# Performance work log

Hardware: AMD Instinct MI355X
Metric: run time of the kernel (lower is better)

## Reference

```python
import jax, jax.numpy as jnp
import numpy as np

N_MODELS = 16
IN_F = 1024
OUT_F = 1024
N_TOK = 8192


def setup_inputs() -> dict:
    key = jax.random.key(0)
    k1, k2, k3, k4 = jax.random.split(key, 4)
    x = jax.random.normal(k1, (N_TOK, IN_F), dtype=jnp.float32)
    idxs = jax.random.randint(k2, (N_TOK,), 0, N_MODELS, dtype=jnp.int64)
    w = jax.random.normal(k3, (N_MODELS, IN_F, OUT_F), dtype=jnp.float32) * 0.02
    b = jax.random.normal(k4, (N_MODELS, OUT_F), dtype=jnp.float32) * 0.02
    return {"x": x, "idxs": idxs, "w": w, "b": b}


def reference(x, idxs, w, b):
    # Equivalent math to the torch loop: for each expert i, tokens with
    # idxs==i get x @ w[i] + b[i]; finally ReLU over all outputs.
    # Loop over the small fixed expert count; selection by mask avoids
    # materializing the [N, E, out] tensor or gathering per-token weights.
    y = jnp.zeros((x.shape[0], w.shape[2]), dtype=x.dtype)
    for i in range(w.shape[0]):
        yi = x @ w[i] + b[i]  # [N, out]
        y = jnp.where((idxs == i)[:, None], yi, y)
    return jax.nn.relu(y)
```

## Files before the change

### kernel.cpp

```cpp
#include <hip/hip_runtime.h>
#include <hip/hip_bf16.h>
#include <stdint.h>

#define N_MODELS 16
#define IN_F 1024
#define OUT_F 1024
#define N_TOK 8192
#define MAX_MT 80

typedef unsigned short u16;
using us4   = __attribute__((ext_vector_type(4))) unsigned short;
using s16x8 = __attribute__((ext_vector_type(8))) short;
using f32x4 = __attribute__((ext_vector_type(4))) float;

__device__ __forceinline__ u16 f2bf(float f) {
    union { float f; uint32_t u; } v;
    v.f = f;
    uint32_t u = v.u;
    u += 0x7fffu + ((u >> 16) & 1u);
    return (u16)(u >> 16);
}

__device__ __forceinline__ void gload16(const u16* g, u16* l) {
    __builtin_amdgcn_global_load_lds(
        (const __attribute__((address_space(1))) void*)g,
        (__attribute__((address_space(3))) void*)l, 16, 0, 0);
}

__global__ void bucket_kernel(const int* __restrict__ idxs,
                              int* __restrict__ perm,
                              int* __restrict__ offs,
                              int* __restrict__ tile_off)
{
    __shared__ int cnt[N_MODELS];
    __shared__ int cur[N_MODELS];
    int t = threadIdx.x;
    if (t < N_MODELS) cnt[t] = 0;
    __syncthreads();
    for (int i = t; i < N_TOK; i += 256) atomicAdd(&cnt[idxs[i]], 1);
    __syncthreads();
    if (t == 0) {
        int o = 0, to = 0;
        for (int e = 0; e < N_MODELS; ++e) {
            offs[e] = o; tile_off[e] = to; cur[e] = o;
            to += (cnt[e] + 127) / 128;
            o  += cnt[e];
        }
        offs[N_MODELS] = o; tile_off[N_MODELS] = to;
    }
    __syncthreads();
    for (int i = t; i < N_TOK; i += 256) {
        int e = idxs[i];
        int p = atomicAdd(&cur[e], 1);
        perm[p] = i;
    }
}

#define WBLOCKS (16*8*16)
#define SH_S 132

__global__ __launch_bounds__(256)
void prep_kernel(const float* __restrict__ w, const float* __restrict__ x,
                 const int* __restrict__ perm, const int* __restrict__ offs,
                 const int* __restrict__ tile_off,
                 u16* __restrict__ wT, u16* __restrict__ xg)
{
    __shared__ u16 sh[64 * SH_S];
    int t  = threadIdx.x;
    int bx = blockIdx.x;

    if (bx < WBLOCKS) {
        int e  = bx >> 7;
        int nt = (bx >> 4) & 7;
        int kg = bx & 15;
        const float* wp = w + (size_t)e * 1048576 + (size_t)kg * 65536 + nt * 128;
        int n4  = t & 31;
        int kr0 = t >> 5;
#pragma unroll
        for (int p = 0; p < 8; ++p) {
            int kr = kr0 + p * 8;
            const float4 v = *(const float4*)(wp + (size_t)kr * 1024 + n4 * 4);
            us4 pk; pk.x = f2bf(v.x); pk.y = f2bf(v.y); pk.z = f2bf(v.z); pk.w = f2bf(v.w);
            *(us4*)(&sh[kr * SH_S + n4 * 4]) = pk;
        }
        __syncthreads();
        int n  = t & 127;
        int qh = t >> 7;
        u16* outb = wT + ((size_t)(e * 8 + nt) * 32) * 4096;
#pragma unroll
        for (int oct = 0; oct < 4; ++oct) {
            int ko = qh + oct * 2;
            int kb = kg * 2 + (ko >> 2);
            int q  = ko & 3;
            s16x8 v;
#pragma unroll
            for (int j = 0; j < 8; ++j) v[j] = (short)sh[(ko * 8 + j) * SH_S + n];
            *(s16x8*)(outb + ((size_t)kb * 4 + q) * 1024 + n * 8) = v;
        }
    } else {
        int bx2 = bx - WBLOCKS;
        int mt = bx2 >> 3;
        int kg = bx2 & 7;
        int total = tile_off[16];
        if (mt >= total) return;
        int e = 0;
        while (tile_off[e + 1] <= mt) ++e;
        int s0   = offs[e] + (mt - tile_off[e]) * 128;
        int sEnd = offs[e + 1];
        int r0   = t >> 3;
        int apos = t & 7;
        int toks[4];
#pragma unroll
        for (int i = 0; i < 4; ++i) {
            int r = r0 + i * 32;
            toks[i] = (s0 + r < sEnd) ? perm[s0 + r] : -1;
        }
        u16* outx = xg + (size_t)mt * 32 * 4096;
        for (int kb4 = 0; kb4 < 4; ++kb4) {
            int kb = kg * 4 + kb4;
#pragma unroll
            for (int i = 0; i < 4; ++i) {
                int r = r0 + i * 32;
                int k = kb * 32 + apos * 4;
                float4 v;
                if (toks[i] >= 0) v = *(const float4*)(x + (size_t)toks[i] * 1024 + k);
                else              v = make_float4(0.f, 0.f, 0.f, 0.f);
                us4 pk; pk.x = f2bf(v.x); pk.y = f2bf(v.y); pk.z = f2bf(v.z); pk.w = f2bf(v.w);
                *(us4*)(&sh[(apos >> 1) * 1024 + r * 8 + (apos & 1) * 4]) = pk;
            }
            __syncthreads();
#pragma unroll
            for (int i = 0; i < 2; ++i) {
                int c = t + i * 256;
                *(s16x8*)(outx + (size_t)kb * 4096 + c * 8) = *(const s16x8*)(&sh[c * 8]);
            }
            __syncthreads();
        }
    }
}

__global__ __launch_bounds__(256)
void gemm_kernel(const u16* __restrict__ xg, const u16* __restrict__ wT,
                 const float* __restrict__ bias,
                 const int* __restrict__ perm, const int* __restrict__ offs,
                 const int* __restrict__ tile_off,
                 float* __restrict__ out)
{
    __shared__ u16 As[4096];
    __shared__ u16 Bs[4096];
    __shared__ int   permS[128];
    __shared__ float biasS[128];
    __shared__ int   toS[N_MODELS + 1];

    int t  = threadIdx.x;
    int bt = blockIdx.y;
    int nt = blockIdx.x;

    if (t <= N_MODELS) toS[t] = tile_off[t];
    __syncthreads();
    if (bt >= toS[N_MODELS]) return;

    int e = 0;
    while (toS[e + 1] <= bt) ++e;
    int s0   = offs[e] + (bt - toS[e]) * 128;
    int sEnd = offs[e + 1];
    int mValid = sEnd - s0; if (mValid > 128) mValid = 128;

    if (t < 128) {
        permS[t] = (s0 + t < sEnd) ? perm[s0 + t] : 0;
        biasS[t] = bias[(size_t)e * OUT_F + nt * 128 + t];
    }

    const u16* atile = xg + (size_t)bt * 32 * 4096;
    const u16* btile = wT + ((size_t)(e * 8 + nt) * 32) * 4096;

    int lane = t & 63;
    int wv   = t >> 6;
    int wm   = (wv >> 1) * 64;
    int wn   = (wv & 1) * 64;
    int m    = lane & 15;
    int q    = lane >> 4;

    f32x4 acc[4][4];
#pragma unroll
    for (int i = 0; i < 4; ++i)
#pragma unroll
        for (int j = 0; j < 4; ++j)
            acc[i][j] = (f32x4){0.f, 0.f, 0.f, 0.f};

    int c = wv * 2;

    for (int kb = 0; kb < 32; ++kb) {
        const u16* ga = atile + kb * 4096;
        const u16* gb = btile + kb * 4096;
        gload16(ga + (c    ) * 512 + lane * 8, &As[(c    ) * 512]);
        gload16(ga + (c + 1) * 512 + lane * 8, &As[(c + 1) * 512]);
        gload16(gb + (c    ) * 512 + lane * 8, &Bs[(c    ) * 512]);
        gload16(gb + (c + 1) * 512 + lane * 8, &Bs[(c + 1) * 512]);
        __syncthreads();

        s16x8 af[4], bf[4];
#pragma unroll
        for (int mt2 = 0; mt2 < 4; ++mt2)
            af[mt2] = *(const s16x8*)(&As[q * 1024 + (wm + mt2 * 16 + m) * 8]);
#pragma unroll
        for (int nt2 = 0; nt2 < 4; ++nt2)
            bf[nt2] = *(const s16x8*)(&Bs[q * 1024 + (wn + nt2 * 16 + m) * 8]);
#pragma unroll
        for (int mt2 = 0; mt2 < 4; ++mt2)
#pragma unroll
            for (int nt2 = 0; nt2 < 4; ++nt2)
                acc[mt2][nt2] = __builtin_amdgcn_mfma_f32_16x16x32_bf16(
                    af[mt2], bf[nt2], acc[mt2][nt2], 0, 0, 0);
        __syncthreads();
    }

#pragma unroll
    for (int mt2 = 0; mt2 < 4; ++mt2) {
        int rbase = wm + mt2 * 16 + q * 4;
#pragma unroll
        for (int i = 0; i < 4; ++i) {
            int r = rbase + i;
            if (r < mValid) {
                int tok = permS[r];
                float* orow = out + (size_t)tok * OUT_F + nt * 128;
#pragma unroll
                for (int nt2 = 0; nt2 < 4; ++nt2) {
                    int col = wn + nt2 * 16 + m;
                    float v = acc[mt2][nt2][i] + biasS[col];
                    orow[col] = v > 0.f ? v : 0.f;
                }
            }
        }
    }
}

extern "C" void kernel_launch(void* const* d_in, const int* in_sizes, int n_in,
                              void* d_out, int out_size, void* d_ws, size_t ws_size,
                              hipStream_t stream) {
    const float* x    = (const float*)d_in[0];
    const int*   idxs = (const int*)d_in[1];
    const float* w    = (const float*)d_in[2];
    const float* b    = (const float*)d_in[3];
    float* out = (float*)d_out;

    u16* wT = (u16*)d_ws;
    u16* xg = wT + (size_t)N_MODELS * IN_F * OUT_F;
    int* perm     = (int*)(xg + (size_t)MAX_MT * 32 * 4096);
    int* offs     = perm + N_TOK;
    int* tile_off = offs + (N_MODELS + 1);

    bucket_kernel<<<1, 256, 0, stream>>>(idxs, perm, offs, tile_off);
    prep_kernel<<<WBLOCKS + 640, 256, 0, stream>>>(w, x, perm, offs, tile_off, wT, xg);
    gemm_kernel<<<dim3(8, MAX_MT), 256, 0, stream>>>(xg, wT, b, perm, offs, tile_off, out);
}
```

Before: 194.5 us.

## Parallelize token bucketing and split weight/activation prep into separate kernels

The single-block bucketing kernel is replaced by a multi-block histogram, a one-thread scan, and a multi-block atomic scatter, spreading the token bucketing across many blocks. The combined prep kernel is split into a weight-conversion kernel, which now reads columns directly without an LDS transpose, and a separate activation-gather kernel. This removes serialization on a single block but adds several extra kernel launches and a memset. The direct strided weight reads may also be less coalesced than the old staged transpose.

```diff
diff --git a/kernel.cpp b/kernel.cpp
--- a/kernel.cpp
+++ b/kernel.cpp
@@ -27,115 +27,103 @@
         (__attribute__((address_space(3))) void*)l, 16, 0, 0);
 }
 
-__global__ void bucket_kernel(const int* __restrict__ idxs,
-                              int* __restrict__ perm,
-                              int* __restrict__ offs,
-                              int* __restrict__ tile_off)
-{
+__global__ void hist_kernel(const int* __restrict__ idxs, int* __restrict__ ghist) {
     __shared__ int cnt[N_MODELS];
-    __shared__ int cur[N_MODELS];
     int t = threadIdx.x;
     if (t < N_MODELS) cnt[t] = 0;
     __syncthreads();
-    for (int i = t; i < N_TOK; i += 256) atomicAdd(&cnt[idxs[i]], 1);
+    int i = blockIdx.x * 256 + t;
+    atomicAdd(&cnt[idxs[i]], 1);
     __syncthreads();
-    if (t == 0) {
+    if (t < N_MODELS) atomicAdd(&ghist[t], cnt[t]);
+}
+
+__global__ void scan_kernel(const int* __restrict__ ghist,
+                            int* __restrict__ offs, int* __restrict__ tile_off,
+                            int* __restrict__ gcur) {
+    if (threadIdx.x == 0) {
         int o = 0, to = 0;
         for (int e = 0; e < N_MODELS; ++e) {
-            offs[e] = o; tile_off[e] = to; cur[e] = o;
-            to += (cnt[e] + 127) / 128;
-            o  += cnt[e];
+            offs[e] = o; tile_off[e] = to; gcur[e] = o;
+            to += (ghist[e] + 127) >> 7;
+            o  += ghist[e];
         }
         offs[N_MODELS] = o; tile_off[N_MODELS] = to;
     }
-    __syncthreads();
-    for (int i = t; i < N_TOK; i += 256) {
-        int e = idxs[i];
-        int p = atomicAdd(&cur[e], 1);
-        perm[p] = i;
-    }
-}
-
-#define WBLOCKS (16*8*16)
-#define SH_S 132
+}
+
+__global__ void scatter_kernel(const int* __restrict__ idxs,
+                               int* __restrict__ gcur, int* __restrict__ perm) {
+    int i = blockIdx.x * 256 + threadIdx.x;
+    int e = idxs[i];
+    int p = atomicAdd(&gcur[e], 1);
+    perm[p] = i;
+}
 
 __global__ __launch_bounds__(256)
-void prep_kernel(const float* __restrict__ w, const float* __restrict__ x,
-                 const int* __restrict__ perm, const int* __restrict__ offs,
-                 const int* __restrict__ tile_off,
-                 u16* __restrict__ wT, u16* __restrict__ xg)
-{
-    __shared__ u16 sh[64 * SH_S];
-    int t  = threadIdx.x;
-    int bx = blockIdx.x;
-
-    if (bx < WBLOCKS) {
-        int e  = bx >> 7;
-        int nt = (bx >> 4) & 7;
-        int kg = bx & 15;
-        const float* wp = w + (size_t)e * 1048576 + (size_t)kg * 65536 + nt * 128;
-        int n4  = t & 31;
-        int kr0 = t >> 5;
-#pragma unroll
-        for (int p = 0; p < 8; ++p) {
-            int kr = kr0 + p * 8;
-            const float4 v = *(const float4*)(wp + (size_t)kr * 1024 + n4 * 4);
-            us4 pk; pk.x = f2bf(v.x); pk.y = f2bf(v.y); pk.z = f2bf(v.z); pk.w = f2bf(v.w);
-            *(us4*)(&sh[kr * SH_S + n4 * 4]) = pk;
-        }
-        __syncthreads();
-        int n  = t & 127;
-        int qh = t >> 7;
-        u16* outb = wT + ((size_t)(e * 8 + nt) * 32) * 4096;
-#pragma unroll
-        for (int oct = 0; oct < 4; ++oct) {
-            int ko = qh + oct * 2;
-            int kb = kg * 2 + (ko >> 2);
-            int q  = ko & 3;
-            s16x8 v;
-#pragma unroll
-            for (int j = 0; j < 8; ++j) v[j] = (short)sh[(ko * 8 + j) * SH_S + n];
-            *(s16x8*)(outb + ((size_t)kb * 4 + q) * 1024 + n * 8) = v;
-        }
-    } else {
-        int bx2 = bx - WBLOCKS;
-        int mt = bx2 >> 3;
-        int kg = bx2 & 7;
-        int total = tile_off[16];
-        if (mt >= total) return;
-        int e = 0;
-        while (tile_off[e + 1] <= mt) ++e;
-        int s0   = offs[e] + (mt - tile_off[e]) * 128;
-        int sEnd = offs[e + 1];
-        int r0   = t >> 3;
-        int apos = t & 7;
-        int toks[4];
+void wprep_kernel(const float* __restrict__ w, u16* __restrict__ wT) {
+    int bx  = blockIdx.x;
+    int e   = bx >> 7;
+    int nt  = (bx >> 4) & 7;
+    int kb2 = bx & 15;
+    const float* wp = w + (size_t)e * (IN_F * OUT_F) + (size_t)kb2 * 64 * OUT_F + nt * 128;
+    u16* ob = wT + ((size_t)(e * 8 + nt) * 32 + kb2 * 2) * 4096;
+    int n    = threadIdx.x & 127;
+    int half = threadIdx.x >> 7;
+#pragma unroll
+    for (int i = 0; i < 4; ++i) {
+        int ko = half + i * 2;
+        s16x8 v;
+#pragma unroll
+        for (int j = 0; j < 8; ++j)
+            v[j] = (short)f2bf(wp[(size_t)(ko * 8 + j) * OUT_F + n]);
+        *(s16x8*)(ob + ((size_t)((ko >> 2) * 4 + (ko & 3)) * 128 + n) * 8) = v;
+    }
+}
+
+__global__ __launch_bounds__(256)
+void xprep_kernel(const float* __restrict__ x,
+                  const int* __restrict__ perm, const int* __restrict__ offs,
+                  const int* __restrict__ tile_off, u16* __restrict__ xg) {
+    __shared__ u16 sh[4096];
+    int t   = threadIdx.x;
+    int bx2 = blockIdx.x;
+    int mt  = bx2 >> 3;
+    int kg  = bx2 & 7;
+    int total = tile_off[N_MODELS];
+    if (mt >= total) return;
+    int e = 0;
+    while (tile_off[e + 1] <= mt) ++e;
+    int s0   = offs[e] + (mt - tile_off[e]) * 128;
+    int sEnd = offs[e + 1];
+    int r0   = t >> 3;
+    int apos = t & 7;
+    int toks[4];
+#pragma unroll
+    for (int i = 0; i < 4; ++i) {
+        int r = r0 + i * 32;
+        toks[i] = (s0 + r < sEnd) ? perm[s0 + r] : -1;
+    }
+    u16* outx = xg + (size_t)mt * 32 * 4096;
+    for (int kb4 = 0; kb4 < 4; ++kb4) {
+        int kb = kg * 4 + kb4;
 #pragma unroll
         for (int i = 0; i < 4; ++i) {
             int r = r0 + i * 32;
-            toks[i] = (s0 + r < sEnd) ? perm[s0 + r] : -1;
-        }
-        u16* outx = xg + (size_t)mt * 32 * 4096;
-        for (int kb4 = 0; kb4 < 4; ++kb4) {
-            int kb = kg * 4 + kb4;
-#pragma unroll
-            for (int i = 0; i < 4; ++i) {
-                int r = r0 + i * 32;
-                int k = kb * 32 + apos * 4;
-                float4 v;
-                if (toks[i] >= 0) v = *(const float4*)(x + (size_t)toks[i] * 1024 + k);
-                else              v = make_float4(0.f, 0.f, 0.f, 0.f);
-                us4 pk; pk.x = f2bf(v.x); pk.y = f2bf(v.y); pk.z = f2bf(v.z); pk.w = f2bf(v.w);
-                *(us4*)(&sh[(apos >> 1) * 1024 + r * 8 + (apos & 1) * 4]) = pk;
-            }
-            __syncthreads();
-#pragma unroll
-            for (int i = 0; i < 2; ++i) {
-                int c = t + i * 256;
-                *(s16x8*)(outx + (size_t)kb * 4096 + c * 8) = *(const s16x8*)(&sh[c * 8]);
-            }
-            __syncthreads();
-        }
+            int k = kb * 32 + apos * 4;
+            float4 v;
+            if (toks[i] >= 0) v = *(const float4*)(x + (size_t)toks[i] * IN_F + k);
+            else              v = make_float4(0.f, 0.f, 0.f, 0.f);
+            us4 pk; pk.x = f2bf(v.x); pk.y = f2bf(v.y); pk.z = f2bf(v.z); pk.w = f2bf(v.w);
+            *(us4*)(&sh[(apos >> 1) * 1024 + r * 8 + (apos & 1) * 4]) = pk;
+        }
+        __syncthreads();
+#pragma unroll
+        for (int i = 0; i < 2; ++i) {
+            int c = t + i * 256;
+            *(s16x8*)(outx + (size_t)kb * 4096 + c * 8) = *(const s16x8*)(&sh[c * 8]);
+        }
+        __syncthreads();
     }
 }
 
@@ -249,8 +237,14 @@
     int* perm     = (int*)(xg + (size_t)MAX_MT * 32 * 4096);
     int* offs     = perm + N_TOK;
     int* tile_off = offs + (N_MODELS + 1);
-
-    bucket_kernel<<<1, 256, 0, stream>>>(idxs, perm, offs, tile_off);
-    prep_kernel<<<WBLOCKS + 640, 256, 0, stream>>>(w, x, perm, offs, tile_off, wT, xg);
+    int* ghist    = tile_off + (N_MODELS + 1);
+    int* gcur     = ghist + N_MODELS;
+
+    hipMemsetAsync(ghist, 0, N_MODELS * sizeof(int), stream);
+    hist_kernel<<<N_TOK / 256, 256, 0, stream>>>(idxs, ghist);
+    scan_kernel<<<1, 64, 0, stream>>>(ghist, offs, tile_off, gcur);
+    scatter_kernel<<<N_TOK / 256, 256, 0, stream>>>(idxs, gcur, perm);
+    wprep_kernel<<<16 * 8 * 16, 256, 0, stream>>>(w, wT);
+    xprep_kernel<<<MAX_MT * 8, 256, 0, stream>>>(x, perm, offs, tile_off, xg);
     gemm_kernel<<<dim3(8, MAX_MT), 256, 0, stream>>>(xg, wT, b, perm, offs, tile_off, out);
 }
```

New measurement: 212.0 us. 1.09x slower.
